# Optimization experiments

Measured on AMD Instinct MI355X. Metric: run time of the kernel, lower is better.

Reference implementation:

```python
import jax, jax.numpy as jnp
import numpy as np

D_MODEL = 1024
D_STATE = 16
EXPAND = 2
D_INNER = EXPAND * D_MODEL          # 2048
DT_RANK = D_MODEL // 16             # 64
BATCH = 2
LENGTH = 2048


def setup_inputs() -> dict:
    key = jax.random.key(0)
    ks = jax.random.split(key, 10)
    s = 0.02
    x = jax.random.normal(ks[0], (BATCH, LENGTH, D_MODEL), jnp.float32)
    W_in = jax.random.normal(ks[1], (D_MODEL, 2 * D_INNER), jnp.float32) * s
    b_in = jnp.zeros((2 * D_INNER,), jnp.float32)
    W_x = jax.random.normal(ks[2], (D_INNER, DT_RANK + 2 * D_STATE), jnp.float32) * s
    b_x = jnp.zeros((DT_RANK + 2 * D_STATE,), jnp.float32)
    W_dt = jax.random.normal(ks[3], (DT_RANK, D_INNER), jnp.float32) * s
    b_dt = jnp.zeros((D_INNER,), jnp.float32)
    # A = arange(1..d_state) repeated per channel; A_log = log(A)
    A_log = jnp.log(jnp.tile(jnp.arange(1, D_STATE + 1, dtype=jnp.float32), (D_INNER, 1)))
    D = jnp.ones((D_INNER,), jnp.float32)
    W_out = jax.random.normal(ks[4], (D_INNER, D_MODEL), jnp.float32) * s
    b_out = jnp.zeros((D_MODEL,), jnp.float32)
    return dict(x=x, W_in=W_in, b_in=b_in, W_x=W_x, b_x=b_x,
                W_dt=W_dt, b_dt=b_dt, A_log=A_log, D=D,
                W_out=W_out, b_out=b_out)


def reference(x, W_in, b_in, W_x, b_x, W_dt, b_dt, A_log, D, W_out, b_out):
    b, l, _ = x.shape
    # input projection -> gate split
    xz = x @ W_in + b_in                       # [b, l, 2*d_inner]
    x_inner, z = jnp.split(xz, 2, axis=-1)     # each [b, l, d_inner]

    # depthwise causal conv, kernel = ones(3)/3, left pad 2 (trailing mean of 3)
    xp = jnp.pad(x_inner, ((0, 0), (2, 0), (0, 0)))
    x_conv = (xp[:, 0:l] + xp[:, 1:l + 1] + xp[:, 2:l + 2]) / 3.0
    x_conv = jax.nn.silu(x_conv)

    # SSM parameters per timestep
    x_dbl = x_conv @ W_x + b_x                 # [b, l, dt_rank + 2*d_state]
    dt, Bm, Cm = jnp.split(x_dbl, [DT_RANK, DT_RANK + D_STATE], axis=-1)
    dt = jax.nn.softplus(dt @ W_dt + b_dt)     # [b, l, d_inner]
    A = -jnp.exp(A_log)                        # [d_inner, d_state]

    def step(h, inp):
        dt_t, B_t, C_t, x_t = inp              # [b,d], [b,n], [b,n], [b,d]
        dA = jnp.exp(A[None] * dt_t[..., None])            # [b, d, n]
        h = dA * h + (dt_t * x_t)[..., None] * B_t[:, None, :]
        y = jnp.einsum('bdn,bn->bd', h, C_t)
        return h, y

    h0 = jnp.zeros((b, D_INNER, D_STATE), x.dtype)
    seq = (dt.transpose(1, 0, 2), Bm.transpose(1, 0, 2),
           Cm.transpose(1, 0, 2), x_conv.transpose(1, 0, 2))
    _, ys = jax.lax.scan(step, h0, seq)        # ys: [l, b, d_inner]
    y = ys.transpose(1, 0, 2) + x_conv * D

    out = (y * jax.nn.silu(z)) @ W_out + b_out
    return out
```

## Files before the change

kernel.cpp:

```cpp
#include <hip/hip_runtime.h>
#include <hip/hip_bf16.h>

typedef __attribute__((ext_vector_type(8))) short short8;
typedef __attribute__((ext_vector_type(4))) float f32x4;
typedef __attribute__((ext_vector_type(4))) float float4v;

#define NCHUNK 32
#define CT 64

static __device__ __forceinline__ unsigned short f2bf(float f) {
    union { float f; unsigned u; } v; v.f = f;
    unsigned r = v.u + 0x7fff + ((v.u >> 16) & 1);
    return (unsigned short)(r >> 16);
}

static __device__ __forceinline__ void gld16(const unsigned short* g, unsigned short* l) {
    __builtin_amdgcn_global_load_lds(
        (const __attribute__((address_space(1))) void*)g,
        (__attribute__((address_space(3))) void*)l, 16, 0, 0);
}

__global__ __launch_bounds__(256) void cast_bf16(
    const float* __restrict__ in, unsigned short* __restrict__ out, int n8)
{
    int i = blockIdx.x * 256 + threadIdx.x;
    if (i >= n8) return;
    const float4v v0 = *reinterpret_cast<const float4v*>(in + (size_t)i * 8);
    const float4v v1 = *reinterpret_cast<const float4v*>(in + (size_t)i * 8 + 4);
    short8 t;
    t[0] = (short)f2bf(v0[0]); t[1] = (short)f2bf(v0[1]);
    t[2] = (short)f2bf(v0[2]); t[3] = (short)f2bf(v0[3]);
    t[4] = (short)f2bf(v1[0]); t[5] = (short)f2bf(v1[1]);
    t[6] = (short)f2bf(v1[2]); t[7] = (short)f2bf(v1[3]);
    *reinterpret_cast<short8*>(out + (size_t)i * 8) = t;
}

__global__ __launch_bounds__(256) void transpose_bf16(
    const float* __restrict__ in, unsigned short* __restrict__ out, int R, int Cc)
{
    __shared__ float tile[32][33];
    int c0 = blockIdx.x * 32, r0 = blockIdx.y * 32;
    int tx = threadIdx.x, ty = threadIdx.y;
#pragma unroll
    for (int i = 0; i < 32; i += 8) {
        int r = r0 + ty + i, c = c0 + tx;
        tile[ty + i][tx] = (r < R && c < Cc) ? in[(size_t)r * Cc + c] : 0.f;
    }
    __syncthreads();
#pragma unroll
    for (int i = 0; i < 32; i += 8) {
        int c = c0 + ty + i, r = r0 + tx;
        if (c < Cc && r < R) out[(size_t)c * R + r] = f2bf(tile[tx][ty + i]);
    }
}

template <int ACT, bool AUX>
__global__ __launch_bounds__(256) void gemm_bf(
    const unsigned short* __restrict__ A, int lda,
    const unsigned short* __restrict__ Bt, int ldb,
    const float* __restrict__ bias,
    float* __restrict__ C, int ldc,
    unsigned short* __restrict__ Cbf, int ldcbf, int ncbf,
    int N, int K)
{
    __shared__ __align__(16) unsigned short As[128 * 32];
    __shared__ __align__(16) unsigned short Bs[128 * 32];

    const int tid  = threadIdx.x;
    const int lane = tid & 63;
    const int wave = tid >> 6;
    const int g    = lane >> 4;
    const int r16  = lane & 15;
    const int wr   = (wave >> 1) * 64;
    const int wc   = (wave & 1) * 64;
    const int rowBase = blockIdx.y * 128;
    const int colBase = blockIdx.x * 128;

    const int e0 = tid * 8;
    const int e1 = (256 + tid) * 8;
    const int r0 = e0 >> 5, c0 = e0 & 31;
    const int r1 = e1 >> 5, c1 = e1 & 31;
    const unsigned short* a0 = A + (size_t)(rowBase + r0) * lda + c0;
    const unsigned short* a1 = A + (size_t)(rowBase + r1) * lda + c1;
    const unsigned short* b0 = Bt + (size_t)(colBase + r0) * ldb + c0;
    const unsigned short* b1 = Bt + (size_t)(colBase + r1) * ldb + c1;

    f32x4 acc[4][4] = {};

    for (int k0 = 0; k0 < K; k0 += 32) {
        gld16(a0 + k0, As + e0);
        gld16(a1 + k0, As + e1);
        gld16(b0 + k0, Bs + e0);
        gld16(b1 + k0, Bs + e1);
        __syncthreads();

        short8 af[4], bfr[4];
#pragma unroll
        for (int m = 0; m < 4; ++m)
            af[m] = *reinterpret_cast<const short8*>(&As[(wr + m * 16 + r16) * 32 + g * 8]);
#pragma unroll
        for (int n = 0; n < 4; ++n)
            bfr[n] = *reinterpret_cast<const short8*>(&Bs[(wc + n * 16 + r16) * 32 + g * 8]);
#pragma unroll
        for (int m = 0; m < 4; ++m)
#pragma unroll
            for (int n = 0; n < 4; ++n)
                acc[m][n] = __builtin_amdgcn_mfma_f32_16x16x32_bf16(
                    af[m], bfr[n], acc[m][n], 0, 0, 0);
        __syncthreads();
    }

#pragma unroll
    for (int m = 0; m < 4; ++m) {
#pragma unroll
        for (int v = 0; v < 4; ++v) {
            int gr = rowBase + wr + m * 16 + g * 4 + v;
#pragma unroll
            for (int n = 0; n < 4; ++n) {
                int gc = colBase + wc + n * 16 + r16;
                if (gc >= N) continue;
                float val = acc[m][n][v] + bias[gc];
                if (ACT == 1) val = (val > 20.f) ? val : log1pf(expf(val));
                C[(size_t)gr * ldc + gc] = val;
                if (AUX && gc < ncbf)
                    Cbf[(size_t)gr * ldcbf + gc] = f2bf(val);
            }
        }
    }
}

template <int ACT>
__global__ __launch_bounds__(256) void gemm_mfma(
    const float* __restrict__ A, int lda,
    const unsigned short* __restrict__ Bt, int ldb,
    const float* __restrict__ bias,
    float* __restrict__ C, int ldc,
    int M, int N, int K)
{
    __shared__ unsigned short As[128 * 32];
    __shared__ unsigned short Bs[128 * 32];

    const int tid  = threadIdx.x;
    const int lane = tid & 63;
    const int wave = tid >> 6;
    const int g    = lane >> 4;
    const int r16  = lane & 15;
    const int wr   = (wave >> 1) * 64;
    const int wc   = (wave & 1) * 64;
    const int rowBase = blockIdx.y * 128;
    const int colBase = blockIdx.x * 128;

    f32x4 acc[4][4] = {};

    for (int k0 = 0; k0 < K; k0 += 32) {
#pragma unroll
        for (int c = 0; c < 2; ++c) {
            int chunk = c * 256 + tid;
            int r = chunk >> 2, slot = chunk & 3;
            int gr = rowBase + r;
            short8 t = {};
            if (gr < M) {
                const float* src = A + (size_t)gr * lda + k0 + slot * 8;
                float4v v0 = *reinterpret_cast<const float4v*>(src);
                float4v v1 = *reinterpret_cast<const float4v*>(src + 4);
                t[0] = (short)f2bf(v0[0]); t[1] = (short)f2bf(v0[1]);
                t[2] = (short)f2bf(v0[2]); t[3] = (short)f2bf(v0[3]);
                t[4] = (short)f2bf(v1[0]); t[5] = (short)f2bf(v1[1]);
                t[6] = (short)f2bf(v1[2]); t[7] = (short)f2bf(v1[3]);
            }
            int sslot = slot ^ (r & 3);
            *reinterpret_cast<short8*>(&As[r * 32 + sslot * 8]) = t;
        }
#pragma unroll
        for (int c = 0; c < 2; ++c) {
            int chunk = c * 256 + tid;
            int r = chunk >> 2, slot = chunk & 3;
            int gn = colBase + r;
            short8 t = {};
            if (gn < N)
                t = *reinterpret_cast<const short8*>(Bt + (size_t)gn * ldb + k0 + slot * 8);
            int sslot = slot ^ (r & 3);
            *reinterpret_cast<short8*>(&Bs[r * 32 + sslot * 8]) = t;
        }
        __syncthreads();

        short8 af[4], bfr[4];
#pragma unroll
        for (int m = 0; m < 4; ++m) {
            int r = wr + m * 16 + r16;
            af[m] = *reinterpret_cast<const short8*>(&As[r * 32 + (g ^ (r & 3)) * 8]);
        }
#pragma unroll
        for (int n = 0; n < 4; ++n) {
            int r = wc + n * 16 + r16;
            bfr[n] = *reinterpret_cast<const short8*>(&Bs[r * 32 + (g ^ (r & 3)) * 8]);
        }
#pragma unroll
        for (int m = 0; m < 4; ++m)
#pragma unroll
            for (int n = 0; n < 4; ++n)
                acc[m][n] = __builtin_amdgcn_mfma_f32_16x16x32_bf16(
                    af[m], bfr[n], acc[m][n], 0, 0, 0);
        __syncthreads();
    }

#pragma unroll
    for (int m = 0; m < 4; ++m) {
#pragma unroll
        for (int v = 0; v < 4; ++v) {
            int gr = rowBase + wr + m * 16 + g * 4 + v;
            if (gr >= M) continue;
#pragma unroll
            for (int n = 0; n < 4; ++n) {
                int gc = colBase + wc + n * 16 + r16;
                if (gc >= N) continue;
                float val = acc[m][n][v] + bias[gc];
                if (ACT == 1) val = (val > 20.f) ? val : log1pf(expf(val));
                C[(size_t)gr * ldc + gc] = val;
            }
        }
    }
}

template <bool BF>
__global__ __launch_bounds__(256) void conv_silu(
    const float* __restrict__ xz, float* __restrict__ xconv,
    unsigned short* __restrict__ xconv_bf)
{
    int idx = blockIdx.x * blockDim.x + threadIdx.x;
    if (idx >= 4096 * 2048) return;
    int d = idx & 2047;
    int row = idx >> 11;
    int l = row & 2047;

    float s = xz[(size_t)row * 4096 + d];
    if (l >= 1) s += xz[(size_t)(row - 1) * 4096 + d];
    if (l >= 2) s += xz[(size_t)(row - 2) * 4096 + d];
    s *= (1.f / 3.f);
    float sv = s / (1.f + __expf(-s));
    xconv[idx] = sv;
    if (BF) xconv_bf[idx] = f2bf(sv);
}


__global__ __launch_bounds__(256) void scan_passA(
    const float* __restrict__ dt,
    const float* __restrict__ xdbl,
    const float* __restrict__ xconv,
    const float* __restrict__ A_log,
    float* __restrict__ Pc,
    float* __restrict__ Sc)
{
    __shared__ float sBC[CT][32];
    const int tid  = threadIdx.x;
    const int bid  = blockIdx.x;
    const int dg   = bid & 31;
    const int c    = (bid >> 5) & 31;
    const int b    = bid >> 10;
    const int lane = tid & 63;
    const int wave = tid >> 6;
    const int chi  = lane & 15;
    const int ng   = lane >> 4;
    const int d    = dg * 64 + wave * 16 + chi;
    const size_t rowBase = (size_t)b * 2048 + (size_t)c * CT;

    for (int i = tid; i < CT * 8; i += 256) {
        int tt = i >> 3, q = i & 7;
        *reinterpret_cast<float4v*>(&sBC[tt][q * 4]) =
            *reinterpret_cast<const float4v*>(&xdbl[(rowBase + tt) * 96 + 64 + q * 4]);
    }
    __syncthreads();

    float4v Aval, h = {}, P = {1.f, 1.f, 1.f, 1.f};
#pragma unroll
    for (int j = 0; j < 4; ++j) Aval[j] = -expf(A_log[d * 16 + ng * 4 + j]);

    const float* pdt = dt + rowBase * 2048 + d;
    const float* px  = xconv + rowBase * 2048 + d;
    float dt_c = *pdt, x_c = *px;
    for (int t = 0; t < CT; ++t) {
        float dt_n = 0.f, x_n = 0.f;
        if (t + 1 < CT) { dt_n = pdt[2048]; x_n = px[2048]; }
        pdt += 2048; px += 2048;

        float4v Bv = *reinterpret_cast<const float4v*>(&sBC[t][ng * 4]);
        float u = dt_c * x_c;
#pragma unroll
        for (int j = 0; j < 4; ++j) {
            float dA = __expf(Aval[j] * dt_c);
            P[j] *= dA;
            h[j] = dA * h[j] + u * Bv[j];
        }
        dt_c = dt_n; x_c = x_n;
    }
    size_t o = (((size_t)(b * NCHUNK + c)) * 2048 + d) * 16 + ng * 4;
    *reinterpret_cast<float4v*>(&Pc[o]) = P;
    *reinterpret_cast<float4v*>(&Sc[o]) = h;
}

__global__ __launch_bounds__(256) void scan_passB(
    float* __restrict__ Pc, const float* __restrict__ Sc)
{
    int idx = blockIdx.x * 256 + threadIdx.x;
    int ng  = idx & 3;
    int d   = (idx >> 2) & 2047;
    int b   = idx >> 13;
    float4v h = {};
#pragma unroll
    for (int c = 0; c < NCHUNK; ++c) {
        size_t o = (((size_t)(b * NCHUNK + c)) * 2048 + d) * 16 + ng * 4;
        float4v Pv = *reinterpret_cast<const float4v*>(&Pc[o]);
        float4v Sv = *reinterpret_cast<const float4v*>(&Sc[o]);
        *reinterpret_cast<float4v*>(&Pc[o]) = h;
#pragma unroll
        for (int j = 0; j < 4; ++j) h[j] = Pv[j] * h[j] + Sv[j];
    }
}

__global__ __launch_bounds__(256) void scan_passC2(
    const float* __restrict__ dt,
    const float* __restrict__ xdbl,
    const float* __restrict__ xz,
    const float* __restrict__ xconv,
    const float* __restrict__ A_log,
    const float* __restrict__ Dp,
    const float* __restrict__ Pc,
    unsigned short* __restrict__ gated_bf)
{
    __shared__ float sBC[CT][32];
    const int tid  = threadIdx.x;
    const int bid  = blockIdx.x;
    const int dg   = bid & 31;
    const int c    = (bid >> 5) & 31;
    const int b    = bid >> 10;
    const int lane = tid & 63;
    const int wave = tid >> 6;
    const int chi  = lane & 15;
    const int ng   = lane >> 4;
    const int d    = dg * 64 + wave * 16 + chi;
    const size_t rowBase = (size_t)b * 2048 + (size_t)c * CT;

    for (int i = tid; i < CT * 8; i += 256) {
        int tt = i >> 3, q = i & 7;
        *reinterpret_cast<float4v*>(&sBC[tt][q * 4]) =
            *reinterpret_cast<const float4v*>(&xdbl[(rowBase + tt) * 96 + 64 + q * 4]);
    }
    __syncthreads();

    float4v Aval;
#pragma unroll
    for (int j = 0; j < 4; ++j) Aval[j] = -expf(A_log[d * 16 + ng * 4 + j]);
    const float Dval = Dp[d];

    float4v h = *reinterpret_cast<const float4v*>(
        &Pc[(((size_t)(b * NCHUNK + c)) * 2048 + d) * 16 + ng * 4]);

    const float* pdt = dt + rowBase * 2048 + d;
    const float* px  = xconv + rowBase * 2048 + d;
    const float* pz  = xz + rowBase * 4096 + 2048 + d;
    unsigned short* pwb = gated_bf + rowBase * 2048 + d;
    float dt_c = *pdt, x_c = *px;

    for (int t = 0; t < CT; ++t) {
        float dt_n = 0.f, x_n = 0.f;
        if (t + 1 < CT) { dt_n = pdt[2048]; x_n = px[2048]; }
        pdt += 2048; px += 2048;

        float4v Bv = *reinterpret_cast<const float4v*>(&sBC[t][ng * 4]);
        float4v Cv = *reinterpret_cast<const float4v*>(&sBC[t][16 + ng * 4]);
        float u = dt_c * x_c;
        float p = 0.f;
#pragma unroll
        for (int j = 0; j < 4; ++j) {
            float dA = __expf(Aval[j] * dt_c);
            h[j] = dA * h[j] + u * Bv[j];
            p += h[j] * Cv[j];
        }
        p += __shfl_xor(p, 16);
        p += __shfl_xor(p, 32);

        if (ng == 0) {
            float y = p + x_c * Dval;
            float zv = *pz;
            float sz = zv / (1.f + __expf(-zv));
            *pwb = f2bf(y * sz);
        }
        pz += 4096; pwb += 2048;
        dt_c = dt_n; x_c = x_n;
    }
}

__global__ __launch_bounds__(256) void scan_kernel(
    const float* __restrict__ dt, const float* __restrict__ xdbl,
    const float* __restrict__ xz, float* __restrict__ xconv,
    const float* __restrict__ A_log, const float* __restrict__ Dp)
{
    const int L = 2048, DI = 2048;
    const int n = threadIdx.x & 15;
    const int chi = threadIdx.x >> 4;
    const int b = blockIdx.x / 128;
    const int d = (blockIdx.x % 128) * 16 + chi;

    const float Aval = -expf(A_log[d * 16 + n]);
    const float Dval = Dp[d];
    float h = 0.f;
    const size_t rowBase = (size_t)b * L;

    float dt_c = dt[rowBase * DI + d];
    float x_c  = xconv[rowBase * DI + d];
    float B_c  = xdbl[rowBase * 96 + 64 + n];
    float C_c  = xdbl[rowBase * 96 + 80 + n];

    for (int t = 0; t < L; ++t) {
        size_t row = rowBase + t;
        float dt_n = 0.f, x_n = 0.f, B_n = 0.f, C_n = 0.f;
        if (t + 1 < L) {
            size_t rn = row + 1;
            dt_n = dt[rn * DI + d];
            x_n  = xconv[rn * DI + d];
            B_n  = xdbl[rn * 96 + 64 + n];
            C_n  = xdbl[rn * 96 + 80 + n];
        }
        float dA = __expf(Aval * dt_c);
        h = dA * h + (dt_c * x_c) * B_c;
        float p = h * C_c;
        p += __shfl_xor(p, 1, 16);
        p += __shfl_xor(p, 2, 16);
        p += __shfl_xor(p, 4, 16);
        p += __shfl_xor(p, 8, 16);
        if (n == 0) {
            float y = p + x_c * Dval;
            float zv = xz[row * 4096 + 2048 + d];
            float sz = zv / (1.f + __expf(-zv));
            xconv[row * DI + d] = y * sz;
        }
        dt_c = dt_n; x_c = x_n; B_c = B_n; C_c = C_n;
    }
}

extern "C" void kernel_launch(void* const* d_in, const int* in_sizes, int n_in,
                              void* d_out, int out_size, void* d_ws, size_t ws_size,
                              hipStream_t stream)
{
    const float* x     = (const float*)d_in[0];
    const float* W_in  = (const float*)d_in[1];
    const float* b_in  = (const float*)d_in[2];
    const float* W_x   = (const float*)d_in[3];
    const float* b_x   = (const float*)d_in[4];
    const float* W_dt  = (const float*)d_in[5];
    const float* b_dt  = (const float*)d_in[6];
    const float* A_log = (const float*)d_in[7];
    const float* Dp    = (const float*)d_in[8];
    const float* W_out = (const float*)d_in[9];
    const float* b_out = (const float*)d_in[10];
    float* out = (float*)d_out;

    float* ws    = (float*)d_ws;
    float* xz    = ws;
    float* xconv = xz + 16777216;
    float* xdbl  = xconv + 8388608;
    float* dtbuf = xdbl + 393216;
    float* Pc    = dtbuf + 8388608;
    float* Sc    = Pc + 2097152;

    const size_t base_f32 = 16777216 + 8388608 + 393216 + 8388608;
    const size_t wshorts  = 4096 * 1024 + 96 * 2048 + 2048 * 64 + 1024 * 2048;
    const size_t bfshorts = 4096 * 1024 + 8388608 + 4096 * 64;
    const size_t needed_t1 = (base_f32 + 2 * 2097152) * 4 + (wshorts + bfshorts) * 2;
    const size_t needed_t2 = base_f32 * 4 + wshorts * 2;

    const int tier = (ws_size >= needed_t1) ? 1 : (ws_size >= needed_t2) ? 2 : 0;
    if (tier == 0) return;

    unsigned short* wbuf = (tier == 1) ? (unsigned short*)(Sc + 2097152)
                                       : (unsigned short*)Pc;
    unsigned short* WinT  = wbuf;
    unsigned short* WxT   = WinT  + 4096 * 1024;
    unsigned short* WdtT  = WxT   + 96 * 2048;
    unsigned short* WoutT = WdtT  + 2048 * 64;
    unsigned short* x_bf     = WoutT + 1024 * 2048;
    unsigned short* xconv_bf = x_bf + 4096 * 1024;
    unsigned short* xdbl_bf  = xconv_bf + 8388608;
    unsigned short* gated_bf = xconv_bf;

    dim3 tblk(32, 8);
    transpose_bf16<<<dim3(128, 32), tblk, 0, stream>>>(W_in, WinT, 1024, 4096);
    transpose_bf16<<<dim3(3, 64),   tblk, 0, stream>>>(W_x,  WxT,  2048, 96);
    transpose_bf16<<<dim3(64, 2),   tblk, 0, stream>>>(W_dt, WdtT, 64, 2048);
    transpose_bf16<<<dim3(32, 64),  tblk, 0, stream>>>(W_out,WoutT,2048, 1024);

    dim3 blk(256);

    if (tier == 1) {
        cast_bf16<<<2048, blk, 0, stream>>>(x, x_bf, 4096 * 1024 / 8);

        gemm_bf<0, false><<<dim3(32, 32), blk, 0, stream>>>(
            x_bf, 1024, WinT, 1024, b_in, xz, 4096, nullptr, 0, 0, 4096, 1024);

        conv_silu<true><<<(4096 * 2048 + 255) / 256, blk, 0, stream>>>(
            xz, xconv, xconv_bf);

        gemm_bf<0, true><<<dim3(1, 32), blk, 0, stream>>>(
            xconv_bf, 2048, WxT, 2048, b_x, xdbl, 96, xdbl_bf, 64, 64, 96, 2048);

        gemm_bf<1, false><<<dim3(16, 32), blk, 0, stream>>>(
            xdbl_bf, 64, WdtT, 64, b_dt, dtbuf, 2048, nullptr, 0, 0, 2048, 64);

        scan_passA<<<2048, blk, 0, stream>>>(dtbuf, xdbl, xconv, A_log, Pc, Sc);
        scan_passB<<<64, blk, 0, stream>>>(Pc, Sc);
        scan_passC2<<<2048, blk, 0, stream>>>(
            dtbuf, xdbl, xz, xconv, A_log, Dp, Pc, gated_bf);

        gemm_bf<0, false><<<dim3(8, 32), blk, 0, stream>>>(
            gated_bf, 2048, WoutT, 2048, b_out, out, 1024, nullptr, 0, 0, 1024, 2048);
    } else {
        gemm_mfma<0><<<dim3(32, 32), blk, 0, stream>>>(
            x, 1024, WinT, 1024, b_in, xz, 4096, 4096, 4096, 1024);
        conv_silu<false><<<(4096 * 2048 + 255) / 256, blk, 0, stream>>>(
            xz, xconv, nullptr);
        gemm_mfma<0><<<dim3(1, 32), blk, 0, stream>>>(
            xconv, 2048, WxT, 2048, b_x, xdbl, 96, 4096, 96, 2048);
        gemm_mfma<1><<<dim3(16, 32), blk, 0, stream>>>(
            xdbl, 96, WdtT, 64, b_dt, dtbuf, 2048, 4096, 2048, 64);
        scan_kernel<<<256, blk, 0, stream>>>(dtbuf, xdbl, xz, xconv, A_log, Dp);
        gemm_mfma<0><<<dim3(8, 32), blk, 0, stream>>>(
            xconv, 2048, WoutT, 2048, b_out, out, 1024, 4096, 1024, 2048);
    }
}
```

Baseline: 457.9 us.

## Double-buffer GEMM LDS, split-K the x-projection, recompute conv in scan

The bf16 GEMM now double-buffers its LDS tiles so the next K-slice loads while MFMAs run. The narrow W_x projection becomes a 4-way split-K with a separate combine kernel that adds the bias and writes the bf16 copy. The fp32 xconv buffer is no longer written in the main path; both scan passes recompute the causal mean and silu from xz. This trades extra global reads of xz and one extra launch for less memory traffic and better occupancy of the small GEMM.

```diff
diff --git a/kernel.cpp b/kernel.cpp
--- a/kernel.cpp
+++ b/kernel.cpp
@@ -54,17 +54,16 @@
     }
 }
 
-template <int ACT, bool AUX>
+template <int ACT, bool PART>
 __global__ __launch_bounds__(256) void gemm_bf(
     const unsigned short* __restrict__ A, int lda,
     const unsigned short* __restrict__ Bt, int ldb,
     const float* __restrict__ bias,
     float* __restrict__ C, int ldc,
-    unsigned short* __restrict__ Cbf, int ldcbf, int ncbf,
-    int N, int K)
-{
-    __shared__ __align__(16) unsigned short As[128 * 32];
-    __shared__ __align__(16) unsigned short Bs[128 * 32];
+    int N, int kLen, size_t partStride)
+{
+    __shared__ __align__(16) unsigned short As[2][128 * 32];
+    __shared__ __align__(16) unsigned short Bs[2][128 * 32];
 
     const int tid  = threadIdx.x;
     const int lane = tid & 63;
@@ -74,33 +73,44 @@
     const int wr   = (wave >> 1) * 64;
     const int wc   = (wave & 1) * 64;
     const int rowBase = blockIdx.y * 128;
-    const int colBase = blockIdx.x * 128;
+    const int colBase = PART ? 0 : blockIdx.x * 128;
+    const int kOff    = PART ? blockIdx.x * kLen : 0;
+    if (PART) C += partStride * blockIdx.x;
 
     const int e0 = tid * 8;
     const int e1 = (256 + tid) * 8;
     const int r0 = e0 >> 5, c0 = e0 & 31;
     const int r1 = e1 >> 5, c1 = e1 & 31;
-    const unsigned short* a0 = A + (size_t)(rowBase + r0) * lda + c0;
-    const unsigned short* a1 = A + (size_t)(rowBase + r1) * lda + c1;
-    const unsigned short* b0 = Bt + (size_t)(colBase + r0) * ldb + c0;
-    const unsigned short* b1 = Bt + (size_t)(colBase + r1) * ldb + c1;
+    const unsigned short* a0 = A + (size_t)(rowBase + r0) * lda + c0 + kOff;
+    const unsigned short* a1 = A + (size_t)(rowBase + r1) * lda + c1 + kOff;
+    const unsigned short* b0 = Bt + (size_t)(colBase + r0) * ldb + c0 + kOff;
+    const unsigned short* b1 = Bt + (size_t)(colBase + r1) * ldb + c1 + kOff;
 
     f32x4 acc[4][4] = {};
 
-    for (int k0 = 0; k0 < K; k0 += 32) {
-        gld16(a0 + k0, As + e0);
-        gld16(a1 + k0, As + e1);
-        gld16(b0 + k0, Bs + e0);
-        gld16(b1 + k0, Bs + e1);
-        __syncthreads();
-
+    gld16(a0, As[0] + e0);
+    gld16(a1, As[0] + e1);
+    gld16(b0, Bs[0] + e0);
+    gld16(b1, Bs[0] + e1);
+    __syncthreads();
+
+    const int nSteps = kLen >> 5;
+    int cur = 0;
+    for (int s = 0; s < nSteps; ++s) {
+        if (s + 1 < nSteps) {
+            int ko = (s + 1) * 32;
+            gld16(a0 + ko, As[cur ^ 1] + e0);
+            gld16(a1 + ko, As[cur ^ 1] + e1);
+            gld16(b0 + ko, Bs[cur ^ 1] + e0);
+            gld16(b1 + ko, Bs[cur ^ 1] + e1);
+        }
         short8 af[4], bfr[4];
 #pragma unroll
         for (int m = 0; m < 4; ++m)
-            af[m] = *reinterpret_cast<const short8*>(&As[(wr + m * 16 + r16) * 32 + g * 8]);
+            af[m] = *reinterpret_cast<const short8*>(&As[cur][(wr + m * 16 + r16) * 32 + g * 8]);
 #pragma unroll
         for (int n = 0; n < 4; ++n)
-            bfr[n] = *reinterpret_cast<const short8*>(&Bs[(wc + n * 16 + r16) * 32 + g * 8]);
+            bfr[n] = *reinterpret_cast<const short8*>(&Bs[cur][(wc + n * 16 + r16) * 32 + g * 8]);
 #pragma unroll
         for (int m = 0; m < 4; ++m)
 #pragma unroll
@@ -108,6 +118,7 @@
                 acc[m][n] = __builtin_amdgcn_mfma_f32_16x16x32_bf16(
                     af[m], bfr[n], acc[m][n], 0, 0, 0);
         __syncthreads();
+        cur ^= 1;
     }
 
 #pragma unroll
@@ -119,14 +130,30 @@
             for (int n = 0; n < 4; ++n) {
                 int gc = colBase + wc + n * 16 + r16;
                 if (gc >= N) continue;
-                float val = acc[m][n][v] + bias[gc];
-                if (ACT == 1) val = (val > 20.f) ? val : log1pf(expf(val));
+                float val = acc[m][n][v];
+                if (!PART) {
+                    val += bias[gc];
+                    if (ACT == 1) val = (val > 20.f) ? val : log1pf(expf(val));
+                }
                 C[(size_t)gr * ldc + gc] = val;
-                if (AUX && gc < ncbf)
-                    Cbf[(size_t)gr * ldcbf + gc] = f2bf(val);
             }
         }
     }
+}
+
+__global__ __launch_bounds__(256) void combine3(
+    const float* __restrict__ Cpart, const float* __restrict__ b_x,
+    float* __restrict__ xdbl, unsigned short* __restrict__ xdbl_bf)
+{
+    int idx = blockIdx.x * 256 + threadIdx.x;
+    if (idx >= 4096 * 96) return;
+    const int S = 4096 * 96;
+    float v = Cpart[idx] + Cpart[idx + S] + Cpart[idx + 2 * S] + Cpart[idx + 3 * S];
+    int row = idx / 96;
+    int col = idx - row * 96;
+    v += b_x[col];
+    xdbl[idx] = v;
+    if (col < 64) xdbl_bf[row * 64 + col] = f2bf(v);
 }
 
 template <int ACT>
@@ -222,7 +249,7 @@
     }
 }
 
-template <bool BF>
+template <int MODE>
 __global__ __launch_bounds__(256) void conv_silu(
     const float* __restrict__ xz, float* __restrict__ xconv,
     unsigned short* __restrict__ xconv_bf)
@@ -238,18 +265,99 @@
     if (l >= 2) s += xz[(size_t)(row - 2) * 4096 + d];
     s *= (1.f / 3.f);
     float sv = s / (1.f + __expf(-s));
-    xconv[idx] = sv;
-    if (BF) xconv_bf[idx] = f2bf(sv);
+    if (MODE == 0) xconv[idx] = sv;
+    else           xconv_bf[idx] = f2bf(sv);
 }
 
 
 __global__ __launch_bounds__(256) void scan_passA(
     const float* __restrict__ dt,
     const float* __restrict__ xdbl,
-    const float* __restrict__ xconv,
+    const float* __restrict__ xz,
     const float* __restrict__ A_log,
     float* __restrict__ Pc,
     float* __restrict__ Sc)
+{
+    __shared__ float sB[CT][16];
+    const int tid  = threadIdx.x;
+    const int bid  = blockIdx.x;
+    const int dg   = bid & 31;
+    const int c    = (bid >> 5) & 31;
+    const int b    = bid >> 10;
+    const int lane = tid & 63;
+    const int wave = tid >> 6;
+    const int chi  = lane & 15;
+    const int ng   = lane >> 4;
+    const int d    = dg * 64 + wave * 16 + chi;
+    const size_t rowBase = (size_t)b * 2048 + (size_t)c * CT;
+
+    for (int i = tid; i < CT * 4; i += 256) {
+        int tt = i >> 2, q = i & 3;
+        *reinterpret_cast<float4v*>(&sB[tt][q * 4]) =
+            *reinterpret_cast<const float4v*>(&xdbl[(rowBase + tt) * 96 + 64 + q * 4]);
+    }
+    __syncthreads();
+
+    float4v Aval, h = {}, P = {1.f, 1.f, 1.f, 1.f};
+#pragma unroll
+    for (int j = 0; j < 4; ++j) Aval[j] = -expf(A_log[d * 16 + ng * 4 + j]);
+
+    const float* pdt = dt + rowBase * 2048 + d;
+    const float* pxz = xz + rowBase * 4096 + d;
+    float w2 = 0.f, w1 = 0.f;
+    if (c > 0) { w2 = pxz[-2 * 4096]; w1 = pxz[-4096]; }
+    float dt_c = *pdt, curx = *pxz;
+
+    for (int t = 0; t < CT; ++t) {
+        float dt_n = 0.f, cur_n = 0.f;
+        if (t + 1 < CT) { dt_n = pdt[2048]; cur_n = pxz[4096]; }
+        pdt += 2048; pxz += 4096;
+
+        float s = (w2 + w1 + curx) * (1.f / 3.f);
+        float x_c = s / (1.f + __expf(-s));
+
+        float4v Bv = *reinterpret_cast<const float4v*>(&sB[t][ng * 4]);
+        float u = dt_c * x_c;
+#pragma unroll
+        for (int j = 0; j < 4; ++j) {
+            float dA = __expf(Aval[j] * dt_c);
+            P[j] *= dA;
+            h[j] = dA * h[j] + u * Bv[j];
+        }
+        w2 = w1; w1 = curx; curx = cur_n; dt_c = dt_n;
+    }
+    size_t o = (((size_t)(b * NCHUNK + c)) * 2048 + d) * 16 + ng * 4;
+    *reinterpret_cast<float4v*>(&Pc[o]) = P;
+    *reinterpret_cast<float4v*>(&Sc[o]) = h;
+}
+
+__global__ __launch_bounds__(256) void scan_passB(
+    float* __restrict__ Pc, const float* __restrict__ Sc)
+{
+    int idx = blockIdx.x * 256 + threadIdx.x;
+    int ng  = idx & 3;
+    int d   = (idx >> 2) & 2047;
+    int b   = idx >> 13;
+    float4v h = {};
+#pragma unroll
+    for (int c = 0; c < NCHUNK; ++c) {
+        size_t o = (((size_t)(b * NCHUNK + c)) * 2048 + d) * 16 + ng * 4;
+        float4v Pv = *reinterpret_cast<const float4v*>(&Pc[o]);
+        float4v Sv = *reinterpret_cast<const float4v*>(&Sc[o]);
+        *reinterpret_cast<float4v*>(&Pc[o]) = h;
+#pragma unroll
+        for (int j = 0; j < 4; ++j) h[j] = Pv[j] * h[j] + Sv[j];
+    }
+}
+
+__global__ __launch_bounds__(256) void scan_passC2(
+    const float* __restrict__ dt,
+    const float* __restrict__ xdbl,
+    const float* __restrict__ xz,
+    const float* __restrict__ A_log,
+    const float* __restrict__ Dp,
+    const float* __restrict__ Pc,
+    unsigned short* __restrict__ gated_bf)
 {
     __shared__ float sBC[CT][32];
     const int tid  = threadIdx.x;
@@ -271,82 +379,6 @@
     }
     __syncthreads();
 
-    float4v Aval, h = {}, P = {1.f, 1.f, 1.f, 1.f};
-#pragma unroll
-    for (int j = 0; j < 4; ++j) Aval[j] = -expf(A_log[d * 16 + ng * 4 + j]);
-
-    const float* pdt = dt + rowBase * 2048 + d;
-    const float* px  = xconv + rowBase * 2048 + d;
-    float dt_c = *pdt, x_c = *px;
-    for (int t = 0; t < CT; ++t) {
-        float dt_n = 0.f, x_n = 0.f;
-        if (t + 1 < CT) { dt_n = pdt[2048]; x_n = px[2048]; }
-        pdt += 2048; px += 2048;
-
-        float4v Bv = *reinterpret_cast<const float4v*>(&sBC[t][ng * 4]);
-        float u = dt_c * x_c;
-#pragma unroll
-        for (int j = 0; j < 4; ++j) {
-            float dA = __expf(Aval[j] * dt_c);
-            P[j] *= dA;
-            h[j] = dA * h[j] + u * Bv[j];
-        }
-        dt_c = dt_n; x_c = x_n;
-    }
-    size_t o = (((size_t)(b * NCHUNK + c)) * 2048 + d) * 16 + ng * 4;
-    *reinterpret_cast<float4v*>(&Pc[o]) = P;
-    *reinterpret_cast<float4v*>(&Sc[o]) = h;
-}
-
-__global__ __launch_bounds__(256) void scan_passB(
-    float* __restrict__ Pc, const float* __restrict__ Sc)
-{
-    int idx = blockIdx.x * 256 + threadIdx.x;
-    int ng  = idx & 3;
-    int d   = (idx >> 2) & 2047;
-    int b   = idx >> 13;
-    float4v h = {};
-#pragma unroll
-    for (int c = 0; c < NCHUNK; ++c) {
-        size_t o = (((size_t)(b * NCHUNK + c)) * 2048 + d) * 16 + ng * 4;
-        float4v Pv = *reinterpret_cast<const float4v*>(&Pc[o]);
-        float4v Sv = *reinterpret_cast<const float4v*>(&Sc[o]);
-        *reinterpret_cast<float4v*>(&Pc[o]) = h;
-#pragma unroll
-        for (int j = 0; j < 4; ++j) h[j] = Pv[j] * h[j] + Sv[j];
-    }
-}
-
-__global__ __launch_bounds__(256) void scan_passC2(
-    const float* __restrict__ dt,
-    const float* __restrict__ xdbl,
-    const float* __restrict__ xz,
-    const float* __restrict__ xconv,
-    const float* __restrict__ A_log,
-    const float* __restrict__ Dp,
-    const float* __restrict__ Pc,
-    unsigned short* __restrict__ gated_bf)
-{
-    __shared__ float sBC[CT][32];
-    const int tid  = threadIdx.x;
-    const int bid  = blockIdx.x;
-    const int dg   = bid & 31;
-    const int c    = (bid >> 5) & 31;
-    const int b    = bid >> 10;
-    const int lane = tid & 63;
-    const int wave = tid >> 6;
-    const int chi  = lane & 15;
-    const int ng   = lane >> 4;
-    const int d    = dg * 64 + wave * 16 + chi;
-    const size_t rowBase = (size_t)b * 2048 + (size_t)c * CT;
-
-    for (int i = tid; i < CT * 8; i += 256) {
-        int tt = i >> 3, q = i & 7;
-        *reinterpret_cast<float4v*>(&sBC[tt][q * 4]) =
-            *reinterpret_cast<const float4v*>(&xdbl[(rowBase + tt) * 96 + 64 + q * 4]);
-    }
-    __syncthreads();
-
     float4v Aval;
 #pragma unroll
     for (int j = 0; j < 4; ++j) Aval[j] = -expf(A_log[d * 16 + ng * 4 + j]);
@@ -356,15 +388,20 @@
         &Pc[(((size_t)(b * NCHUNK + c)) * 2048 + d) * 16 + ng * 4]);
 
     const float* pdt = dt + rowBase * 2048 + d;
-    const float* px  = xconv + rowBase * 2048 + d;
+    const float* pxz = xz + rowBase * 4096 + d;
     const float* pz  = xz + rowBase * 4096 + 2048 + d;
     unsigned short* pwb = gated_bf + rowBase * 2048 + d;
-    float dt_c = *pdt, x_c = *px;
+    float w2 = 0.f, w1 = 0.f;
+    if (c > 0) { w2 = pxz[-2 * 4096]; w1 = pxz[-4096]; }
+    float dt_c = *pdt, curx = *pxz;
 
     for (int t = 0; t < CT; ++t) {
-        float dt_n = 0.f, x_n = 0.f;
-        if (t + 1 < CT) { dt_n = pdt[2048]; x_n = px[2048]; }
-        pdt += 2048; px += 2048;
+        float dt_n = 0.f, cur_n = 0.f;
+        if (t + 1 < CT) { dt_n = pdt[2048]; cur_n = pxz[4096]; }
+        pdt += 2048; pxz += 4096;
+
+        float s = (w2 + w1 + curx) * (1.f / 3.f);
+        float x_c = s / (1.f + __expf(-s));
 
         float4v Bv = *reinterpret_cast<const float4v*>(&sBC[t][ng * 4]);
         float4v Cv = *reinterpret_cast<const float4v*>(&sBC[t][16 + ng * 4]);
@@ -386,7 +423,7 @@
             *pwb = f2bf(y * sz);
         }
         pz += 4096; pwb += 2048;
-        dt_c = dt_n; x_c = x_n;
+        w2 = w1; w1 = curx; curx = cur_n; dt_c = dt_n;
     }
 }
 
@@ -462,17 +499,19 @@
     float* dtbuf = xdbl + 393216;
     float* Pc    = dtbuf + 8388608;
     float* Sc    = Pc + 2097152;
+    float* Cpart = Sc + 2097152;
 
     const size_t base_f32 = 16777216 + 8388608 + 393216 + 8388608;
     const size_t wshorts  = 4096 * 1024 + 96 * 2048 + 2048 * 64 + 1024 * 2048;
     const size_t bfshorts = 4096 * 1024 + 8388608 + 4096 * 64;
-    const size_t needed_t1 = (base_f32 + 2 * 2097152) * 4 + (wshorts + bfshorts) * 2;
+    const size_t needed_t1 = (base_f32 + 2 * 2097152 + 1572864) * 4
+                           + (wshorts + bfshorts) * 2;
     const size_t needed_t2 = base_f32 * 4 + wshorts * 2;
 
     const int tier = (ws_size >= needed_t1) ? 1 : (ws_size >= needed_t2) ? 2 : 0;
     if (tier == 0) return;
 
-    unsigned short* wbuf = (tier == 1) ? (unsigned short*)(Sc + 2097152)
+    unsigned short* wbuf = (tier == 1) ? (unsigned short*)(Cpart + 1572864)
                                        : (unsigned short*)Pc;
     unsigned short* WinT  = wbuf;
     unsigned short* WxT   = WinT  + 4096 * 1024;
@@ -495,28 +534,30 @@
         cast_bf16<<<2048, blk, 0, stream>>>(x, x_bf, 4096 * 1024 / 8);
 
         gemm_bf<0, false><<<dim3(32, 32), blk, 0, stream>>>(
-            x_bf, 1024, WinT, 1024, b_in, xz, 4096, nullptr, 0, 0, 4096, 1024);
-
-        conv_silu<true><<<(4096 * 2048 + 255) / 256, blk, 0, stream>>>(
-            xz, xconv, xconv_bf);
-
-        gemm_bf<0, true><<<dim3(1, 32), blk, 0, stream>>>(
-            xconv_bf, 2048, WxT, 2048, b_x, xdbl, 96, xdbl_bf, 64, 64, 96, 2048);
+            x_bf, 1024, WinT, 1024, b_in, xz, 4096, 4096, 1024, 0);
+
+        conv_silu<1><<<(4096 * 2048 + 255) / 256, blk, 0, stream>>>(
+            xz, nullptr, xconv_bf);
+
+        gemm_bf<0, true><<<dim3(4, 32), blk, 0, stream>>>(
+            xconv_bf, 2048, WxT, 2048, nullptr, Cpart, 96, 96, 512,
+            (size_t)4096 * 96);
+        combine3<<<1536, blk, 0, stream>>>(Cpart, b_x, xdbl, xdbl_bf);
 
         gemm_bf<1, false><<<dim3(16, 32), blk, 0, stream>>>(
-            xdbl_bf, 64, WdtT, 64, b_dt, dtbuf, 2048, nullptr, 0, 0, 2048, 64);
-
-        scan_passA<<<2048, blk, 0, stream>>>(dtbuf, xdbl, xconv, A_log, Pc, Sc);
+            xdbl_bf, 64, WdtT, 64, b_dt, dtbuf, 2048, 2048, 64, 0);
+
+        scan_passA<<<2048, blk, 0, stream>>>(dtbuf, xdbl, xz, A_log, Pc, Sc);
         scan_passB<<<64, blk, 0, stream>>>(Pc, Sc);
         scan_passC2<<<2048, blk, 0, stream>>>(
-            dtbuf, xdbl, xz, xconv, A_log, Dp, Pc, gated_bf);
+            dtbuf, xdbl, xz, A_log, Dp, Pc, gated_bf);
 
         gemm_bf<0, false><<<dim3(8, 32), blk, 0, stream>>>(
-            gated_bf, 2048, WoutT, 2048, b_out, out, 1024, nullptr, 0, 0, 1024, 2048);
+            gated_bf, 2048, WoutT, 2048, b_out, out, 1024, 1024, 2048, 0);
     } else {
         gemm_mfma<0><<<dim3(32, 32), blk, 0, stream>>>(
             x, 1024, WinT, 1024, b_in, xz, 4096, 4096, 4096, 1024);
-        conv_silu<false><<<(4096 * 2048 + 255) / 256, blk, 0, stream>>>(
+        conv_silu<0><<<(4096 * 2048 + 255) / 256, blk, 0, stream>>>(
             xz, xconv, nullptr);
         gemm_mfma<0><<<dim3(1, 32), blk, 0, stream>>>(
             xconv, 2048, WxT, 2048, b_x, xdbl, 96, 4096, 96, 2048);
```

Measured after the change: 440.2 us. 3.9% less time.
